# Performance work log

Hardware: AMD Instinct MI355X
Metric: run time of the kernel (lower is better)

The kernel has to match this reference:

```python
import jax, jax.numpy as jnp
import numpy as np

# ---- sedenion multiplication table via Cayley-Dickson construction ----
def _cd_conj(x):
    if x.shape[0] == 1:
        return x
    h = x.shape[0] // 2
    return np.concatenate([_cd_conj(x[:h]), -x[h:]])

def _cd_mult(x, y):
    n = x.shape[0]
    if n == 1:
        return x * y
    h = n // 2
    a, b = x[:h], x[h:]
    c, d = y[:h], y[h:]
    return np.concatenate([
        _cd_mult(a, c) - _cd_mult(_cd_conj(d), b),
        _cd_mult(d, a) + _cd_mult(b, _cd_conj(c)),
    ])

def _sed_table():
    T = np.zeros((16, 16, 16), dtype=np.float32)
    I = np.eye(16, dtype=np.float32)
    for i in range(16):
        for j in range(16):
            r = _cd_mult(I[i], I[j])  # e_i * e_j = sign * e_k
            k = int(np.abs(r).argmax())
            T[i, j, k] = r[k]
    return T

_T = jnp.asarray(_sed_table())  # [16,16,16] constant sign table

DIM = 128
MLP_RATIO = 4
EPS = 1e-5

def _ln(x, g, b):
    m = jnp.mean(x, axis=-1, keepdims=True)
    v = jnp.mean((x - m) ** 2, axis=-1, keepdims=True)
    return (x - m) * jax.lax.rsqrt(v + EPS) * g + b

def setup_inputs() -> dict:
    key = jax.random.key(0)
    ks = jax.random.split(key, 8)
    C, Ch = DIM, DIM * MLP_RATIO
    s = 1.0 / np.sqrt(C)
    inp = {
        "x": jax.random.normal(ks[0], (8, C, 128, 128), dtype=jnp.float32),
        "gamma1": jnp.ones((C,), jnp.float32),
        "beta1": jnp.zeros((C,), jnp.float32),
        "sed_w": jax.random.normal(ks[1], (16, C, C), jnp.float32) * (s / 4.0),
        "w_proj": jax.random.normal(ks[2], (C, C), jnp.float32) * s,
        "b_proj": jnp.zeros((C,), jnp.float32),
        "gamma2": jnp.ones((C,), jnp.float32),
        "beta2": jnp.zeros((C,), jnp.float32),
        "w1": jax.random.normal(ks[3], (C, Ch), jnp.float32) * s,
        "b1": jnp.zeros((Ch,), jnp.float32),
        "w2": jax.random.normal(ks[4], (Ch, C), jnp.float32) * (1.0 / np.sqrt(Ch)),
        "b2": jnp.zeros((C,), jnp.float32),
    }
    return inp

def reference(x, gamma1, beta1, sed_w, w_proj, b_proj, gamma2, beta2, w1, b1, w2, b2):
    B, C, H, W = x.shape  # H, W divisible by 4 -> no padding branch
    h, w = H // 4, W // 4
    xt = jnp.transpose(x, (0, 2, 3, 1))          # [B,H,W,C]
    # norm1
    xn = _ln(xt, gamma1, beta1)
    # window partition: 'b c (h s1)(w s2) -> b h w (s1 s2 c)'
    xw = xn.reshape(B, h, 4, w, 4, C).transpose(0, 1, 3, 2, 4, 5).reshape(B, h, w, 16, C)
    # SedenionLinear: y_k = sum_{i,j} T[i,j,k] * x_i @ W_j  (bias=False)
    ys = jnp.einsum('bhwic,ijk,jcd->bhwkd', xw, _T, sed_w)
    # reverse window + to bhwc
    y = ys.reshape(B, h, w, 4, 4, C).transpose(0, 1, 3, 2, 4, 5).reshape(B, H, W, C)
    # act + proj
    y = jax.nn.gelu(y, approximate=False)
    y = y @ w_proj + b_proj
    # residual 1
    y = xt + y
    # norm2 + MLP + residual 2
    m = _ln(y, gamma2, beta2)
    m = jax.nn.gelu(m @ w1 + b1, approximate=False)
    m = m @ w2 + b2
    out = y + m
    return jnp.transpose(out, (0, 3, 1, 2))  # back to [B,C,H,W]
```

## Files before the change

### kernel.cpp

```cpp
#include <hip/hip_runtime.h>
#include <hip/hip_bf16.h>

#define DEVI __device__ __forceinline__

typedef __attribute__((ext_vector_type(8))) __bf16 bf16x8;
typedef __attribute__((ext_vector_type(4))) __bf16 bf16x4;
typedef __attribute__((ext_vector_type(4))) float f32x4;

using bf16 = __hip_bfloat16;

DEVI float bf2f(bf16 v) { return __bfloat162float(v); }
DEVI bf16 f2bf(float v) { return __float2bfloat16(v); }

DEVI float gelu_fast(float v) {
    float t = v * (2.30220777f + 0.10294322f * v * v);
    float e = __builtin_amdgcn_exp2f(t);
    return v - v * __builtin_amdgcn_rcpf(e + 1.0f);
}

DEVI void async16(void* lds, const void* g) {
    __builtin_amdgcn_global_load_lds(
        (const __attribute__((address_space(1))) void*)g,
        (__attribute__((address_space(3))) void*)lds, 16, 0, 0);
}

DEVI int cd_sign(int i, int j) {
    int s = 1, n = 16;
    while (n > 1) {
        int h = n >> 1;
        int ih = (i >= h), jh = (j >= h);
        if (!ih && !jh) {
        } else if (!ih && jh) {
            int ni = j - h, nj = i;
            i = ni; j = nj;
        } else if (ih && !jh) {
            if (j != 0) s = -s;
            i = i - h;
        } else {
            int ni = j - h, nj = i - h;
            if (ni == 0) s = -s;
            i = ni; j = nj;
        }
        n = h;
    }
    return s;
}

__global__ __launch_bounds__(256) void k_prep_A(const float* __restrict__ sed_w,
                                                bf16* __restrict__ At) {
    __shared__ float tile[128][129];
    int bi = blockIdx.x;
    int i = bi >> 4, k = bi & 15;
    int j = i ^ k;
    float s = (float)cd_sign(i, j);
    int t = threadIdx.x;
    int lo = t & 127, hi = t >> 7;
    const float* src = sed_w + j * 16384;
    for (int it = 0; it < 64; ++it) {
        int c = it * 2 + hi;
        tile[c][lo] = src[c * 128 + lo];
    }
    __syncthreads();
    for (int it = 0; it < 64; ++it) {
        int d = it * 2 + hi;
        At[(long)(k * 128 + d) * 2048 + i * 128 + lo] = f2bf(s * tile[lo][d]);
    }
}

__global__ __launch_bounds__(256) void k_prep_w(const float* __restrict__ wp,
                                                const float* __restrict__ w1,
                                                const float* __restrict__ w2,
                                                bf16* __restrict__ wpT,
                                                bf16* __restrict__ w1T,
                                                bf16* __restrict__ w2T) {
    int idx = blockIdx.x * 256 + threadIdx.x;
    if (idx < 16384) {
        int d = idx >> 7, c = idx & 127;
        wpT[idx] = f2bf(wp[c * 128 + d]);
    } else if (idx < 16384 + 65536) {
        int e = idx - 16384;
        int o = e >> 7, c = e & 127;
        w1T[e] = f2bf(w1[c * 512 + o]);
    } else if (idx < 16384 + 131072) {
        int e = idx - 81920;
        int o = e >> 9, c = e & 511;
        w2T[e] = f2bf(w2[c * 128 + o]);
    }
}

__global__ __launch_bounds__(256) void k_ln1(const float* __restrict__ x,
                                             const float* __restrict__ g,
                                             const float* __restrict__ bta,
                                             bf16* __restrict__ xt,
                                             bf16* __restrict__ xn) {
    __shared__ float tile[128][128];
    __shared__ float ps[2][128], pss[2][128];
    int b = blockIdx.x >> 7, r = blockIdx.x & 127;
    int t = threadIdx.x, c = t & 127, half = t >> 7;
    const float* xb = x + ((long)b * 128 * 128 + r) * 128;
    for (int it = 0; it < 64; ++it) {
        int ch = it * 2 + half;
        tile[ch][c] = xb[(long)ch * 16384 + c];
    }
    __syncthreads();
    float s = 0.f, ss = 0.f;
    for (int ch = half * 64; ch < half * 64 + 64; ++ch) {
        float v = tile[ch][c];
        s += v; ss += v * v;
    }
    ps[half][c] = s; pss[half][c] = ss;
    __syncthreads();
    float S = ps[0][c] + ps[1][c], SS = pss[0][c] + pss[1][c];
    float mean = S * (1.f / 128.f);
    float var = SS * (1.f / 128.f) - mean * mean;
    float rstd = rsqrtf(var + 1e-5f);
    long n = (((long)b * 32 + (r >> 2)) * 32 + (c >> 2)) * 16 + ((r & 3) * 4 + (c & 3));
    bf16* xtr = xt + n * 128 + half * 64;
    bf16* xnr = xn + n * 128 + half * 64;
#pragma unroll
    for (int v8 = 0; v8 < 8; ++v8) {
        bf16x8 pt, pn;
#pragma unroll
        for (int e = 0; e < 8; ++e) {
            int ch = half * 64 + v8 * 8 + e;
            float v = tile[ch][c];
            pt[e] = (__bf16)v;
            pn[e] = (__bf16)((v - mean) * rstd * g[ch] + bta[ch]);
        }
        *(bf16x8*)&xtr[v8 * 8] = pt;
        *(bf16x8*)&xnr[v8 * 8] = pn;
    }
}

__global__ __launch_bounds__(256, 3) void k_gemm_sed(const bf16* __restrict__ At,
                                                     const bf16* __restrict__ xn,
                                                     bf16* __restrict__ g_) {
    const int K = 2048;
    __shared__ __align__(16) char buf[34816];
    bf16* lA = (bf16*)buf;
    bf16* lB = (bf16*)(buf + 8192);
    bf16* sOut = (bf16*)buf;
    int t = threadIdx.x;
    long bm = (long)blockIdx.y * 128;
    long bn = (long)blockIdx.x * 128;
    int lane = t & 63;
    int wm = ((t >> 7) & 1) * 64;
    int wn = ((t >> 6) & 1) * 64;
    int l15 = lane & 15, quad = lane >> 4;

    f32x4 acc[4][4] = {};

    int rowA = t >> 2;
    int seg = (t & 3) * 8;
    const bf16* gA = At + (bm + rowA) * (long)K + seg;
    const bf16* gB = xn + (bn + rowA) * (long)K + seg;

    for (int k0 = 0; k0 < K; k0 += 32) {
        async16(&lA[t * 8], gA + k0);
        async16(&lA[2048 + t * 8], gA + (long)64 * K + k0);
        async16(&lB[t * 8], gB + k0);
        async16(&lB[2048 + t * 8], gB + (long)64 * K + k0);
        __syncthreads();
        bf16x8 af[4], bfr[4];
#pragma unroll
        for (int tm = 0; tm < 4; ++tm)
            af[tm] = *(const bf16x8*)&lA[(wm + tm * 16 + l15) * 32 + quad * 8];
#pragma unroll
        for (int tn = 0; tn < 4; ++tn)
            bfr[tn] = *(const bf16x8*)&lB[(wn + tn * 16 + l15) * 32 + quad * 8];
#pragma unroll
        for (int tm = 0; tm < 4; ++tm)
#pragma unroll
            for (int tn = 0; tn < 4; ++tn)
                acc[tm][tn] = __builtin_amdgcn_mfma_f32_16x16x32_bf16(
                    af[tm], bfr[tn], acc[tm][tn], 0, 0, 0);
        __syncthreads();
    }

#pragma unroll
    for (int tn = 0; tn < 4; ++tn) {
        int win = wn + tn * 16 + l15;
#pragma unroll
        for (int tm = 0; tm < 4; ++tm) {
            int kd = wm + tm * 16 + quad * 4;
            bf16x4 p;
#pragma unroll
            for (int reg = 0; reg < 4; ++reg)
                p[reg] = (__bf16)gelu_fast(acc[tm][tn][reg]);
            *(bf16x4*)&sOut[win * 136 + kd] = p;
        }
    }
    __syncthreads();
#pragma unroll
    for (int it = 0; it < 8; ++it) {
        int id = it * 256 + t;
        int win = id >> 4, sg = id & 15;
        bf16x8 v = *(const bf16x8*)&sOut[win * 136 + sg * 8];
        *(bf16x8*)&g_[(bn + win) * 2048 + bm + sg * 8] = v;
    }
}

__global__ __launch_bounds__(256, 3) void k_tail(
    const bf16* __restrict__ g_,
    const bf16* __restrict__ wpT,
    const float* __restrict__ bproj,
    const bf16* __restrict__ xt,
    const float* __restrict__ gamma2, const float* __restrict__ beta2,
    const bf16* __restrict__ w1T,
    const float* __restrict__ b1,
    const bf16* __restrict__ w2T,
    const float* __restrict__ b2,
    float* __restrict__ out)
{
    __shared__ __align__(16) char buf[53248];
    bf16* mpT = (bf16*)buf;
    bf16* hT = (bf16*)(buf + 34816);
    float* stats = (float*)(buf + 34816);
    float* outF = (float*)buf;

    int t = threadIdx.x;
    long tb = (long)blockIdx.x * 128;
    int lane = t & 63;
    int wm = ((t >> 7) & 1) * 64;
    int wm1 = ((t >> 7) & 1) * 32;
    int wn = ((t >> 6) & 1) * 64;
    int l15 = lane & 15, quad = lane >> 4;
    int half = wm >> 6;

    int tok[4];
#pragma unroll
    for (int tn = 0; tn < 4; ++tn) tok[tn] = wn + tn * 16 + l15;

    f32x4 acc1[4][4] = {};
#pragma unroll
    for (int k0 = 0; k0 < 128; k0 += 32) {
        bf16x8 af[4], bfr[4];
#pragma unroll
        for (int tm = 0; tm < 4; ++tm)
            af[tm] = *(const bf16x8*)&wpT[(wm + tm * 16 + l15) * 128 + k0 + quad * 8];
#pragma unroll
        for (int tn = 0; tn < 4; ++tn)
            bfr[tn] = *(const bf16x8*)&g_[(tb + tok[tn]) * 128 + k0 + quad * 8];
#pragma unroll
        for (int tm = 0; tm < 4; ++tm)
#pragma unroll
            for (int tn = 0; tn < 4; ++tn)
                acc1[tm][tn] = __builtin_amdgcn_mfma_f32_16x16x32_bf16(
                    af[tm], bfr[tn], acc1[tm][tn], 0, 0, 0);
    }

#pragma unroll
    for (int tm = 0; tm < 4; ++tm) {
        int c0 = wm + tm * 16 + quad * 4;
        float4 bp = *(const float4*)&bproj[c0];
#pragma unroll
        for (int tn = 0; tn < 4; ++tn) {
            bf16x4 xv = *(const bf16x4*)&xt[(tb + tok[tn]) * 128 + c0];
#pragma unroll
            for (int reg = 0; reg < 4; ++reg)
                acc1[tm][tn][reg] += ((const float*)&bp)[reg] + (float)xv[reg];
        }
    }

#pragma unroll
    for (int tn = 0; tn < 4; ++tn) {
        float s = 0.f, ss = 0.f;
#pragma unroll
        for (int tm = 0; tm < 4; ++tm)
#pragma unroll
            for (int reg = 0; reg < 4; ++reg) {
                float v = acc1[tm][tn][reg];
                s += v; ss += v * v;
            }
        s += __shfl_xor(s, 16); ss += __shfl_xor(ss, 16);
        s += __shfl_xor(s, 32); ss += __shfl_xor(ss, 32);
        if (quad == 0) {
            stats[tok[tn] * 2 + half] = s;
            stats[256 + tok[tn] * 2 + half] = ss;
        }
    }
    __syncthreads();

    float mean[4], rstd[4];
#pragma unroll
    for (int tn = 0; tn < 4; ++tn) {
        float S = stats[tok[tn] * 2] + stats[tok[tn] * 2 + 1];
        float SS = stats[256 + tok[tn] * 2] + stats[256 + tok[tn] * 2 + 1];
        mean[tn] = S * (1.f / 128.f);
        float var = SS * (1.f / 128.f) - mean[tn] * mean[tn];
        rstd[tn] = rsqrtf(var + 1e-5f);
    }
#pragma unroll
    for (int tm = 0; tm < 4; ++tm) {
        int c0 = wm + tm * 16 + quad * 4;
        float4 gv = *(const float4*)&gamma2[c0];
        float4 bv = *(const float4*)&beta2[c0];
#pragma unroll
        for (int tn = 0; tn < 4; ++tn) {
            bf16x4 p;
#pragma unroll
            for (int reg = 0; reg < 4; ++reg)
                p[reg] = (__bf16)((acc1[tm][tn][reg] - mean[tn]) * rstd[tn] *
                                      ((const float*)&gv)[reg] +
                                  ((const float*)&bv)[reg]);
            *(bf16x4*)&mpT[tok[tn] * 136 + c0] = p;
        }
    }
    __syncthreads();

    f32x4 acc2[4][4];
#pragma unroll
    for (int tm = 0; tm < 4; ++tm)
#pragma unroll
        for (int tn = 0; tn < 4; ++tn)
            acc2[tm][tn] = acc1[tm][tn];

    for (int oh = 0; oh < 8; ++oh) {
        f32x4 acch[2][4] = {};
#pragma unroll
        for (int k0 = 0; k0 < 128; k0 += 32) {
            bf16x8 af[2], bfr[4];
#pragma unroll
            for (int tm = 0; tm < 2; ++tm)
                af[tm] = *(const bf16x8*)&w1T[(oh * 64 + wm1 + tm * 16 + l15) * 128 +
                                              k0 + quad * 8];
#pragma unroll
            for (int tn = 0; tn < 4; ++tn)
                bfr[tn] = *(const bf16x8*)&mpT[tok[tn] * 136 + k0 + quad * 8];
#pragma unroll
            for (int tm = 0; tm < 2; ++tm)
#pragma unroll
                for (int tn = 0; tn < 4; ++tn)
                    acch[tm][tn] = __builtin_amdgcn_mfma_f32_16x16x32_bf16(
                        af[tm], bfr[tn], acch[tm][tn], 0, 0, 0);
        }
        __syncthreads();
#pragma unroll
        for (int tm = 0; tm < 2; ++tm) {
            int hc0 = wm1 + tm * 16 + quad * 4;
            float4 bh = *(const float4*)&b1[oh * 64 + hc0];
#pragma unroll
            for (int tn = 0; tn < 4; ++tn) {
                bf16x4 p;
#pragma unroll
                for (int reg = 0; reg < 4; ++reg)
                    p[reg] = (__bf16)gelu_fast(acch[tm][tn][reg] +
                                               ((const float*)&bh)[reg]);
                *(bf16x4*)&hT[tok[tn] * 72 + hc0] = p;
            }
        }
        __syncthreads();
#pragma unroll
        for (int k0 = 0; k0 < 64; k0 += 32) {
            bf16x8 af[4], bfr[4];
#pragma unroll
            for (int tm = 0; tm < 4; ++tm)
                af[tm] = *(const bf16x8*)&w2T[(wm + tm * 16 + l15) * 512 +
                                              oh * 64 + k0 + quad * 8];
#pragma unroll
            for (int tn = 0; tn < 4; ++tn)
                bfr[tn] = *(const bf16x8*)&hT[tok[tn] * 72 + k0 + quad * 8];
#pragma unroll
            for (int tm = 0; tm < 4; ++tm)
#pragma unroll
                for (int tn = 0; tn < 4; ++tn)
                    acc2[tm][tn] = __builtin_amdgcn_mfma_f32_16x16x32_bf16(
                        af[tm], bfr[tn], acc2[tm][tn], 0, 0, 0);
        }
    }
    __syncthreads();

    long win0 = tb >> 4;
    int b = (int)(win0 >> 10);
    int hq = (int)(win0 >> 5) & 31;
    int wq0 = (int)win0 & 31;
#pragma unroll
    for (int p = 0; p < 2; ++p) {
#pragma unroll
        for (int tmi = 0; tmi < 2; ++tmi) {
            int tm = p * 2 + tmi;
            int c0 = wm + tm * 16 + quad * 4;
            int slot0 = (wm >> 1) + tmi * 16 + quad * 4;
            float4 bv = *(const float4*)&b2[c0];
#pragma unroll
            for (int tn = 0; tn < 4; ++tn)
#pragma unroll
                for (int reg = 0; reg < 4; ++reg)
                    outF[(slot0 + reg) * 132 + tok[tn]] =
                        acc2[tm][tn][reg] + ((const float*)&bv)[reg];
        }
        __syncthreads();
#pragma unroll
        for (int it = 0; it < 8; ++it) {
            int id = it * 256 + t;
            int slot = id >> 5, rem = id & 31;
            int rr = rem >> 3, wqo = rem & 7;
            int c = slot + ((slot >= 32) ? 32 : 0) + p * 32;
            f32x4 v = *(const f32x4*)&outF[slot * 132 + wqo * 16 + rr * 4];
            long addr = (((long)b * 128 + c) * 128 + hq * 4 + rr) * 128 +
                        (wq0 + wqo) * 4;
            *(f32x4*)&out[addr] = v;
        }
        __syncthreads();
    }
}

extern "C" void kernel_launch(void* const* d_in, const int* in_sizes, int n_in,
                              void* d_out, int out_size, void* d_ws, size_t ws_size,
                              hipStream_t stream) {
    const float* x      = (const float*)d_in[0];
    const float* gamma1 = (const float*)d_in[1];
    const float* beta1  = (const float*)d_in[2];
    const float* sed_w  = (const float*)d_in[3];
    const float* w_proj = (const float*)d_in[4];
    const float* b_proj = (const float*)d_in[5];
    const float* gamma2 = (const float*)d_in[6];
    const float* beta2  = (const float*)d_in[7];
    const float* w1     = (const float*)d_in[8];
    const float* b1     = (const float*)d_in[9];
    const float* w2     = (const float*)d_in[10];
    const float* b2     = (const float*)d_in[11];

    char* ws = (char*)d_ws;
    bf16* At  = (bf16*)(ws + 0);
    bf16* wpT = (bf16*)(ws + 8388608);
    bf16* w1T = (bf16*)(ws + 8421376);
    bf16* w2T = (bf16*)(ws + 8552448);
    bf16* xt  = (bf16*)(ws + 8683520);
    bf16* xn  = (bf16*)(ws + 42237952);
    bf16* g_  = (bf16*)(ws + 75792384);

    hipLaunchKernelGGL(k_prep_w, dim3(576), dim3(256), 0, stream,
                       w_proj, w1, w2, wpT, w1T, w2T);
    hipLaunchKernelGGL(k_prep_A, dim3(256), dim3(256), 0, stream, sed_w, At);
    hipLaunchKernelGGL(k_ln1, dim3(1024), dim3(256), 0, stream,
                       x, gamma1, beta1, xt, xn);
    hipLaunchKernelGGL(k_gemm_sed, dim3(64, 16), dim3(256), 0, stream,
                       At, xn, g_);
    hipLaunchKernelGGL(k_tail, dim3(1024), dim3(256), 0, stream,
                       g_, wpT, b_proj, xt, gamma2, beta2,
                       w1T, b1, w2T, b2, (float*)d_out);
}
```

Before: 375.5 us.

## Split tail kernel work across 8 waves instead of 4

The fused proj+LN2+MLP tail kernel now runs 512 threads per block, with each wave owning 32 output channels instead of 64. This halves per-wave accumulator register pressure, and the LN statistics reduction and output staging are reworked for four channel groups. The aim is more waves in flight to hide latency of the global weight loads and MFMA chains. The cost is more redundant B-fragment loads per block, and LDS use (53KB per block) may cap how many blocks fit per CU.

```diff
diff --git a/kernel.cpp b/kernel.cpp
--- a/kernel.cpp
+++ b/kernel.cpp
@@ -200,7 +200,7 @@
     }
 }
 
-__global__ __launch_bounds__(256, 3) void k_tail(
+__global__ __launch_bounds__(512, 4) void k_tail(
     const bf16* __restrict__ g_,
     const bf16* __restrict__ wpT,
     const float* __restrict__ bproj,
@@ -221,28 +221,28 @@
     int t = threadIdx.x;
     long tb = (long)blockIdx.x * 128;
     int lane = t & 63;
-    int wm = ((t >> 7) & 1) * 64;
-    int wm1 = ((t >> 7) & 1) * 32;
-    int wn = ((t >> 6) & 1) * 64;
+    int wid = t >> 6;
+    int wn = (wid & 1) * 64;
+    int q4 = wid >> 1;
+    int wc = q4 * 32;
     int l15 = lane & 15, quad = lane >> 4;
-    int half = wm >> 6;
 
     int tok[4];
 #pragma unroll
     for (int tn = 0; tn < 4; ++tn) tok[tn] = wn + tn * 16 + l15;
 
-    f32x4 acc1[4][4] = {};
+    f32x4 acc1[2][4] = {};
 #pragma unroll
     for (int k0 = 0; k0 < 128; k0 += 32) {
-        bf16x8 af[4], bfr[4];
-#pragma unroll
-        for (int tm = 0; tm < 4; ++tm)
-            af[tm] = *(const bf16x8*)&wpT[(wm + tm * 16 + l15) * 128 + k0 + quad * 8];
+        bf16x8 af[2], bfr[4];
+#pragma unroll
+        for (int tm = 0; tm < 2; ++tm)
+            af[tm] = *(const bf16x8*)&wpT[(wc + tm * 16 + l15) * 128 + k0 + quad * 8];
 #pragma unroll
         for (int tn = 0; tn < 4; ++tn)
             bfr[tn] = *(const bf16x8*)&g_[(tb + tok[tn]) * 128 + k0 + quad * 8];
 #pragma unroll
-        for (int tm = 0; tm < 4; ++tm)
+        for (int tm = 0; tm < 2; ++tm)
 #pragma unroll
             for (int tn = 0; tn < 4; ++tn)
                 acc1[tm][tn] = __builtin_amdgcn_mfma_f32_16x16x32_bf16(
@@ -250,8 +250,8 @@
     }
 
 #pragma unroll
-    for (int tm = 0; tm < 4; ++tm) {
-        int c0 = wm + tm * 16 + quad * 4;
+    for (int tm = 0; tm < 2; ++tm) {
+        int c0 = wc + tm * 16 + quad * 4;
         float4 bp = *(const float4*)&bproj[c0];
 #pragma unroll
         for (int tn = 0; tn < 4; ++tn) {
@@ -266,7 +266,7 @@
     for (int tn = 0; tn < 4; ++tn) {
         float s = 0.f, ss = 0.f;
 #pragma unroll
-        for (int tm = 0; tm < 4; ++tm)
+        for (int tm = 0; tm < 2; ++tm)
 #pragma unroll
             for (int reg = 0; reg < 4; ++reg) {
                 float v = acc1[tm][tn][reg];
@@ -275,8 +275,8 @@
         s += __shfl_xor(s, 16); ss += __shfl_xor(ss, 16);
         s += __shfl_xor(s, 32); ss += __shfl_xor(ss, 32);
         if (quad == 0) {
-            stats[tok[tn] * 2 + half] = s;
-            stats[256 + tok[tn] * 2 + half] = ss;
+            stats[tok[tn] * 4 + q4] = s;
+            stats[512 + tok[tn] * 4 + q4] = ss;
         }
     }
     __syncthreads();
@@ -284,15 +284,17 @@
     float mean[4], rstd[4];
 #pragma unroll
     for (int tn = 0; tn < 4; ++tn) {
-        float S = stats[tok[tn] * 2] + stats[tok[tn] * 2 + 1];
-        float SS = stats[256 + tok[tn] * 2] + stats[256 + tok[tn] * 2 + 1];
+        float S = stats[tok[tn] * 4] + stats[tok[tn] * 4 + 1] +
+                  stats[tok[tn] * 4 + 2] + stats[tok[tn] * 4 + 3];
+        float SS = stats[512 + tok[tn] * 4] + stats[512 + tok[tn] * 4 + 1] +
+                   stats[512 + tok[tn] * 4 + 2] + stats[512 + tok[tn] * 4 + 3];
         mean[tn] = S * (1.f / 128.f);
         float var = SS * (1.f / 128.f) - mean[tn] * mean[tn];
         rstd[tn] = rsqrtf(var + 1e-5f);
     }
 #pragma unroll
-    for (int tm = 0; tm < 4; ++tm) {
-        int c0 = wm + tm * 16 + quad * 4;
+    for (int tm = 0; tm < 2; ++tm) {
+        int c0 = wc + tm * 16 + quad * 4;
         float4 gv = *(const float4*)&gamma2[c0];
         float4 bv = *(const float4*)&beta2[c0];
 #pragma unroll
@@ -308,43 +310,38 @@
     }
     __syncthreads();
 
-    f32x4 acc2[4][4];
-#pragma unroll
-    for (int tm = 0; tm < 4; ++tm)
+    f32x4 acc2[2][4];
+#pragma unroll
+    for (int tm = 0; tm < 2; ++tm)
 #pragma unroll
         for (int tn = 0; tn < 4; ++tn)
             acc2[tm][tn] = acc1[tm][tn];
 
     for (int oh = 0; oh < 8; ++oh) {
-        f32x4 acch[2][4] = {};
+        f32x4 acch[4] = {};
 #pragma unroll
         for (int k0 = 0; k0 < 128; k0 += 32) {
-            bf16x8 af[2], bfr[4];
-#pragma unroll
-            for (int tm = 0; tm < 2; ++tm)
-                af[tm] = *(const bf16x8*)&w1T[(oh * 64 + wm1 + tm * 16 + l15) * 128 +
-                                              k0 + quad * 8];
+            bf16x8 af, bfr[4];
+            af = *(const bf16x8*)&w1T[(oh * 64 + q4 * 16 + l15) * 128 +
+                                      k0 + quad * 8];
 #pragma unroll
             for (int tn = 0; tn < 4; ++tn)
                 bfr[tn] = *(const bf16x8*)&mpT[tok[tn] * 136 + k0 + quad * 8];
 #pragma unroll
-            for (int tm = 0; tm < 2; ++tm)
-#pragma unroll
-                for (int tn = 0; tn < 4; ++tn)
-                    acch[tm][tn] = __builtin_amdgcn_mfma_f32_16x16x32_bf16(
-                        af[tm], bfr[tn], acch[tm][tn], 0, 0, 0);
-        }
-        __syncthreads();
-#pragma unroll
-        for (int tm = 0; tm < 2; ++tm) {
-            int hc0 = wm1 + tm * 16 + quad * 4;
+            for (int tn = 0; tn < 4; ++tn)
+                acch[tn] = __builtin_amdgcn_mfma_f32_16x16x32_bf16(
+                    af, bfr[tn], acch[tn], 0, 0, 0);
+        }
+        __syncthreads();
+        {
+            int hc0 = q4 * 16 + quad * 4;
             float4 bh = *(const float4*)&b1[oh * 64 + hc0];
 #pragma unroll
             for (int tn = 0; tn < 4; ++tn) {
                 bf16x4 p;
 #pragma unroll
                 for (int reg = 0; reg < 4; ++reg)
-                    p[reg] = (__bf16)gelu_fast(acch[tm][tn][reg] +
+                    p[reg] = (__bf16)gelu_fast(acch[tn][reg] +
                                                ((const float*)&bh)[reg]);
                 *(bf16x4*)&hT[tok[tn] * 72 + hc0] = p;
             }
@@ -352,16 +349,16 @@
         __syncthreads();
 #pragma unroll
         for (int k0 = 0; k0 < 64; k0 += 32) {
-            bf16x8 af[4], bfr[4];
-#pragma unroll
-            for (int tm = 0; tm < 4; ++tm)
-                af[tm] = *(const bf16x8*)&w2T[(wm + tm * 16 + l15) * 512 +
+            bf16x8 af[2], bfr[4];
+#pragma unroll
+            for (int tm = 0; tm < 2; ++tm)
+                af[tm] = *(const bf16x8*)&w2T[(wc + tm * 16 + l15) * 512 +
                                               oh * 64 + k0 + quad * 8];
 #pragma unroll
             for (int tn = 0; tn < 4; ++tn)
                 bfr[tn] = *(const bf16x8*)&hT[tok[tn] * 72 + k0 + quad * 8];
 #pragma unroll
-            for (int tm = 0; tm < 4; ++tm)
+            for (int tm = 0; tm < 2; ++tm)
 #pragma unroll
                 for (int tn = 0; tn < 4; ++tn)
                     acc2[tm][tn] = __builtin_amdgcn_mfma_f32_16x16x32_bf16(
@@ -376,26 +373,28 @@
     int wq0 = (int)win0 & 31;
 #pragma unroll
     for (int p = 0; p < 2; ++p) {
-#pragma unroll
-        for (int tmi = 0; tmi < 2; ++tmi) {
-            int tm = p * 2 + tmi;
-            int c0 = wm + tm * 16 + quad * 4;
-            int slot0 = (wm >> 1) + tmi * 16 + quad * 4;
-            float4 bv = *(const float4*)&b2[c0];
-#pragma unroll
-            for (int tn = 0; tn < 4; ++tn)
-#pragma unroll
-                for (int reg = 0; reg < 4; ++reg)
-                    outF[(slot0 + reg) * 132 + tok[tn]] =
-                        acc2[tm][tn][reg] + ((const float*)&bv)[reg];
-        }
-        __syncthreads();
-#pragma unroll
-        for (int it = 0; it < 8; ++it) {
-            int id = it * 256 + t;
+        if ((q4 >> 1) == p) {
+            int slot_base = (wc & 32);
+#pragma unroll
+            for (int tm = 0; tm < 2; ++tm) {
+                int c0 = wc + tm * 16 + quad * 4;
+                int slot0 = slot_base + tm * 16 + quad * 4;
+                float4 bv = *(const float4*)&b2[c0];
+#pragma unroll
+                for (int tn = 0; tn < 4; ++tn)
+#pragma unroll
+                    for (int reg = 0; reg < 4; ++reg)
+                        outF[(slot0 + reg) * 132 + tok[tn]] =
+                            acc2[tm][tn][reg] + ((const float*)&bv)[reg];
+            }
+        }
+        __syncthreads();
+#pragma unroll
+        for (int it = 0; it < 4; ++it) {
+            int id = it * 512 + t;
             int slot = id >> 5, rem = id & 31;
             int rr = rem >> 3, wqo = rem & 7;
-            int c = slot + ((slot >= 32) ? 32 : 0) + p * 32;
+            int c = p * 64 + slot;
             f32x4 v = *(const f32x4*)&outF[slot * 132 + wqo * 16 + rr * 4];
             long addr = (((long)b * 128 + c) * 128 + hq * 4 + rr) * 128 +
                         (wq0 + wqo) * 4;
@@ -437,7 +436,7 @@
                        x, gamma1, beta1, xt, xn);
     hipLaunchKernelGGL(k_gemm_sed, dim3(64, 16), dim3(256), 0, stream,
                        At, xn, g_);
-    hipLaunchKernelGGL(k_tail, dim3(1024), dim3(256), 0, stream,
+    hipLaunchKernelGGL(k_tail, dim3(1024), dim3(512), 0, stream,
                        g_, wpT, b_proj, xt, gamma2, beta2,
                        w1T, b1, w2T, b2, (float*)d_out);
 }
```

After: 358.8 us. -4.4%, faster.
